# Kernel optimization log

Hardware: AMD Instinct MI355X
Metric: run time of the kernel (lower is better)

Reference implementation:

```python
import jax, jax.numpy as jnp
import numpy as np

PT_SEQ_LEN = 16    # hardcoded hw_seq_len in the module
THETA = 10000.0


def _rope_tables(head_dim):
    # VisionRotaryEmbeddingFast with dim = head_dim // 2, pt_seq_len = ft_seq_len = 16
    d = head_dim // 2                                   # 32
    freqs = 1.0 / (THETA ** (np.arange(0, d, 2, dtype=np.float64) / d))  # (d//2,) = (16,)
    t = np.arange(PT_SEQ_LEN, dtype=np.float64)         # t / ft * pt = arange since ft==pt
    f = np.einsum('i,j->ij', t, freqs)                  # (16, 16)
    f = np.repeat(f, 2, axis=-1)                        # (16, 32)  '... n -> ... (n r)'
    fa = np.broadcast_to(f[:, None, :], (PT_SEQ_LEN, PT_SEQ_LEN, d))
    fb = np.broadcast_to(f[None, :, :], (PT_SEQ_LEN, PT_SEQ_LEN, d))
    full = np.concatenate([fa, fb], axis=-1).reshape(-1, head_dim)  # (256, head_dim)
    return (jnp.asarray(np.cos(full), dtype=jnp.float32),
            jnp.asarray(np.sin(full), dtype=jnp.float32))


def _rotate_half(x):
    # '... (d r) -> ... d r', r=2; (x1, x2) -> (-x2, x1)
    x = x.reshape(*x.shape[:-1], -1, 2)
    x1, x2 = x[..., 0], x[..., 1]
    return jnp.stack((-x2, x1), axis=-1).reshape(*x.shape[:-2], -1)


def _apply_rope(t, cos, sin):
    # t: (B, H, N, hd); cos/sin: (N, hd)
    return t * cos + _rotate_half(t) * sin


def setup_inputs() -> dict:
    key = jax.random.key(0)
    ks = jax.random.split(key, 5)
    B, N, dim, sem = 64, 256, 1024, 768
    return {
        'q': jax.random.normal(ks[0], (B, N, dim), dtype=jnp.float32),
        'kv': jax.random.normal(ks[1], (B, N, sem), dtype=jnp.float32),
        'Wq': jax.random.normal(ks[2], (dim, dim), dtype=jnp.float32) * 0.02,
        'Wkv': jax.random.normal(ks[3], (sem, 2 * dim), dtype=jnp.float32) * 0.02,
        'Wproj': jax.random.normal(ks[4], (dim, dim), dtype=jnp.float32) * 0.02,
        'bproj': jnp.zeros((dim,), dtype=jnp.float32),
    }


def reference(q, kv, Wq, Wkv, Wproj, bproj):
    B, N, C = q.shape
    H = 16
    hd = C // H
    cos, sin = _rope_tables(hd)

    qh = (q @ Wq).reshape(B, N, H, hd).transpose(0, 2, 1, 3)        # (B,H,N,hd)
    kvh = (kv @ Wkv).reshape(B, N, 2, H, hd).transpose(2, 0, 3, 1, 4)
    k, v = kvh[0], kvh[1]                                           # (B,H,N,hd)

    qh = _apply_rope(qh, cos, sin)
    k = _apply_rope(k, cos, sin)

    scale = 1.0 / jnp.sqrt(jnp.float32(hd))  # F.sdpa default scale
    logits = jnp.einsum('bhqd,bhkd->bhqk', qh, k) * scale
    attn = jax.nn.softmax(logits, axis=-1)
    out = jnp.einsum('bhqk,bhkd->bhqd', attn, v)                    # (B,H,N,hd)
    out = out.transpose(0, 2, 1, 3).reshape(B, N, C)
    return out @ Wproj + bproj
```

## Files before the change

### kernel.cpp

```cpp
#include <hip/hip_runtime.h>
#include <hip/hip_bf16.h>
#include <math.h>


typedef unsigned int uint;
typedef __attribute__((ext_vector_type(4)))  short s16x4;
typedef __attribute__((ext_vector_type(8)))  short s16x8;
typedef __attribute__((ext_vector_type(4)))  float f32x4;
typedef __attribute__((ext_vector_type(16))) float f32x16;

#define AS1 __attribute__((address_space(1)))
#define AS3 __attribute__((address_space(3)))

__device__ __forceinline__ short f2bf(float x){
  union{float f;uint u;}v; v.f=x;
  return (short)((v.u + 0x7FFFu + ((v.u>>16)&1u))>>16);
}
__device__ __forceinline__ float bf2f(short s){
  union{float f;uint u;}v; v.u=((uint)(unsigned short)s)<<16; return v.f;
}
__device__ __forceinline__ uint packbf(float a,float b){
  return (uint)(unsigned short)f2bf(a) | ((uint)(unsigned short)f2bf(b)<<16);
}
__device__ __forceinline__ void gl_lds16(const void* g, void* l){
  __builtin_amdgcn_global_load_lds((const AS1 uint*)g, (AS3 uint*)l, 16, 0, 0);
}
__device__ __forceinline__ s16x8 ld16(const short* p){ return *(const s16x8*)p; }

__global__ void k_prep(const void* Wq, const void* Wkv, const void* Wp,
                       const void* bsrc, const void* qsrc, const void* kvsrc,
                       short* WqT, short* WkvT, short* WpT, float* biasF,
                       float* cosT, float* sinT, short* qbf, short* kvbf,
                       int* flag){
  __shared__ int cnt;
  const uint* qw=(const uint*)qsrc;
  if(threadIdx.x==0) cnt=0;
  __syncthreads();
  int c=0;
  for(int i=threadIdx.x;i<2048;i+=256){
    uint e=(qw[i]>>7)&0xFFu;
    if(e>=120u && e<=130u) c++;
  }
  atomicAdd(&cnt,c);
  __syncthreads();
  const int f=(cnt>1024)?0:1;
  if(threadIdx.x==0 && blockIdx.x==0) *flag=f;

  const long S0=16384, S1=S0+1024, S2=S1+131072, S3=S2+196608, S4=S3+131072,
             S5=S4+2097152, S6=S5+1572864;
  const long stride=(long)gridDim.x*blockDim.x;
  for(long idx=(long)blockIdx.x*blockDim.x+threadIdx.x; idx<S6; idx+=stride){
    if(idx<S0){
      int t=(int)idx, n=t>>6, d=t&63;
      int i=n>>4, j=n&15, p=(d&31)>>1;
      double fr=pow(10000.0, -(double)(2*p)/32.0);
      double tt=(d<32)?(double)i:(double)j;
      double a=tt*fr;
      cosT[t]=(float)cos(a); sinT[t]=(float)sin(a);
    } else if(idx<S1){
      int t=(int)(idx-S0);
      biasF[t]= f ? ((const float*)bsrc)[t] : bf2f(((const short*)bsrc)[t]);
    } else if(idx<S4){
      const void* W; short* WT; int K,Nn; long g;
      if(idx<S2){ W=Wq;  WT=WqT;  K=1024; Nn=1024; g=idx-S1; }
      else if(idx<S3){ W=Wkv; WT=WkvT; K=768; Nn=2048; g=idx-S2; }
      else { W=Wp;  WT=WpT;  K=1024; Nn=1024; g=idx-S3; }
      int n=(int)(g%Nn); int k0=(int)(g/Nn)*8;
      s16x8 o;
      #pragma unroll
      for(int j=0;j<8;j++){
        o[j]= f ? f2bf(((const float*)W)[(long)(k0+j)*Nn+n])
                : ((const short*)W)[(long)(k0+j)*Nn+n];
      }
      *(s16x8*)&WT[(long)n*K+k0]=o;
    } else {
      const void* src; short* dst; long i;
      if(idx<S5){ src=qsrc; dst=qbf; i=idx-S4; }
      else { src=kvsrc; dst=kvbf; i=idx-S5; }
      s16x8 o;
      if(f){
        const float4* s=(const float4*)src;
        float4 a=s[i*2], b=s[i*2+1];
        o[0]=f2bf(a.x);o[1]=f2bf(a.y);o[2]=f2bf(a.z);o[3]=f2bf(a.w);
        o[4]=f2bf(b.x);o[5]=f2bf(b.y);o[6]=f2bf(b.z);o[7]=f2bf(b.w);
      }else{
        o=((const s16x8*)src)[i];
      }
      ((s16x8*)dst)[i]=o;
    }
  }
}

#define BAR   __builtin_amdgcn_s_barrier()
#define LGKM0 asm volatile("s_waitcnt lgkmcnt(0)" ::: "memory")
#define VMC4  asm volatile("s_waitcnt vmcnt(4)" ::: "memory")
#define PRIO1 __builtin_amdgcn_s_setprio(1)
#define PRIO0 __builtin_amdgcn_s_setprio(0)

#define MM(H,V,BR) do{ \
  _Pragma("unroll") for(int ks_=0;ks_<4;ks_++){ \
    _Pragma("unroll") for(int mf_=0;mf_<2;mf_++){ \
      acc[(H)*2+mf_][V]=__builtin_amdgcn_mfma_f32_32x32x16_bf16( \
        aR[mf_][ks_],BR[ks_],acc[(H)*2+mf_][V],0,0,0); \
  }} }while(0)

#define HALFIT(BUF,TA,TB) do{ \
  const short* RA=&lds[BUF][0][wm][0]; \
  const short* RB=&lds[BUF][1][0][0]; \
  ldA(RA,0,aR); ldB(RB,0,bR0); stage(0,0,TA); \
  BAR; LGKM0; PRIO1; MM(0,0,bR0); PRIO0; BAR; \
  ldB(RB,1,bR1); stage(0,1,TA); \
  BAR; LGKM0; PRIO1; MM(0,1,bR1); PRIO0; BAR; \
  ldA(RA,1,aR); stage(1,0,TB); \
  BAR; LGKM0; PRIO1; MM(1,1,bR1); PRIO0; BAR; \
  stage(1,1,TB); \
  BAR; PRIO1; MM(1,0,bR0); PRIO0; VMC4; BAR; \
}while(0)

template<int MODE>
__launch_bounds__(512,2)
__global__ void k_gemm8(const short* __restrict__ Aq, const short* __restrict__ Bq,
                        const short* __restrict__ Akv, const short* __restrict__ Bkv,
                        short* __restrict__ out0, short* __restrict__ out1,
                        short* __restrict__ out2,
                        const float* __restrict__ cosT, const float* __restrict__ sinT,
                        const float* __restrict__ bias, const int* __restrict__ flag,
                        void* __restrict__ dout){
  __shared__ __align__(16) short lds[2][2][2][8192];
  const int tid=threadIdx.x, lane=tid&63, wave=tid>>6;
  const int ln31=lane&31, l5=lane>>5;
  const int wm=wave>>2, wn=wave&3;
  int role, tm, tn, Kdim;
  const short *Ag, *Bg;
  if(MODE==1){
    const int nwg=gridDim.x, cpx=nwg>>3;
    const int wg=((int)blockIdx.x&7)*cpx+((int)blockIdx.x>>3);
    role=2; tn=wg&3; tm=wg>>2; Kdim=1024;
    Ag=Aq+(long)tm*256*1024; Bg=Bq+(long)tn*256*1024;
  } else {
    const int xcd=(int)blockIdx.x&7, pos=(int)blockIdx.x>>3;
    if(pos<32){ role=0; int qi=xcd*32+pos; tn=qi&3; tm=qi>>2; Kdim=1024;
      Ag=Aq+(long)tm*256*1024; Bg=Bq+(long)tn*256*1024; }
    else { role=1; int ki=xcd*64+(pos-32); tn=ki&7; tm=ki>>3; Kdim=768;
      Ag=Akv+(long)tm*256*768; Bg=Bkv+(long)tn*256*768; }
  }
  const int NT=Kdim>>6;
  const int fl=(MODE==1)? *flag : 0;
  f32x16 acc[4][2]={};
  s16x8 aR[2][4], bR0[4], bR1[4];

  auto stage=[&](int op,int hf,int kt){
    int ktw=(kt>=NT)?kt-NT:kt;
    const short* G=(op? Bg:Ag)+((long)(hf*128))*Kdim+ktw*64;
    short* R=&lds[kt&1][op][hf][0];
    #pragma unroll
    for(int l=0;l<2;l++){
      int lr=l*64+wave*8+(lane>>3);
      int c=(lane&7)^((lr>>1)&7);
      gl_lds16(G+(long)lr*Kdim+c*8, R+l*4096+wave*512+lane*8);
    }
  };
  auto ldA=[&](const short* R,int h,s16x8 (&a)[2][4]){
    #pragma unroll
    for(int mf=0;mf<2;mf++){
      int lr=h*64+mf*32+ln31;
      int sw=(lr>>1)&7;
      #pragma unroll
      for(int ks=0;ks<4;ks++){
        int slot=(ks*2+l5)^sw;
        a[mf][ks]=*(const s16x8*)&R[lr*64+slot*8];
      }
    }
  };
  auto ldB=[&](const short* R0,int v,s16x8 (&b)[4]){
    int row=wn*64+v*32+ln31;
    const short* R=R0+(row>>7)*8192;
    int lr=row&127;
    int sw=(lr>>1)&7;
    #pragma unroll
    for(int ks=0;ks<4;ks++){
      int slot=(ks*2+l5)^sw;
      b[ks]=*(const s16x8*)&R[lr*64+slot*8];
    }
  };

  stage(1,0,0); stage(1,1,0); stage(0,0,0); stage(0,1,0);
  stage(1,0,1); stage(1,1,1);
  VMC4;
  BAR;

  for(int t=0;t<NT;t+=2){
    HALFIT(0, t+1, t+2);
    HALFIT(1, t+2, t+3);
  }

  const int mb=tm*256+wm*128, nb=tn*256+wn*64;
  #pragma unroll
  for(int mf=0;mf<4;mf++)
  #pragma unroll
  for(int nf=0;nf<2;nf++){
    const int n=nb+nf*32+ln31;
    if(MODE==1){
      float bi=bias[n];
      #pragma unroll
      for(int r=0;r<16;r++){
        int m=mb+mf*32+(r&3)+8*(r>>2)+4*l5;
        float o=acc[mf][nf][r]+bi;
        long idx=((long)m<<10)+n;
        if(fl) ((float*)dout)[idx]=o;
        else   ((short*)dout)[idx]=f2bf(o);
      }
    } else if(role==0){
      int h=n>>6, d=n&63;
      #pragma unroll
      for(int r=0;r<16;r++){
        int m=mb+mf*32+(r&3)+8*(r>>2)+4*l5;
        int b=m>>8, nn=m&255;
        float v=acc[mf][nf][r];
        float part=__shfl_xor(v,1);
        float c=cosT[(nn<<6)+d], s=sinT[(nn<<6)+d];
        float rot=(d&1)?part:-part;
        out0[(((long)(b*16+h)*256+nn)<<6)+d]=f2bf((v*c+rot*s)*0.125f);
      }
    } else {
      if(n<1024){
        int h=(n>>6)&15, d=n&63;
        #pragma unroll
        for(int r=0;r<16;r++){
          int m=mb+mf*32+(r&3)+8*(r>>2)+4*l5;
          int b=m>>8, nn=m&255;
          float v=acc[mf][nf][r];
          float part=__shfl_xor(v,1);
          float c=cosT[(nn<<6)+d], s=sinT[(nn<<6)+d];
          float rot=(d&1)?part:-part;
          out1[(((long)(b*16+h)*256+nn)<<6)+d]=f2bf(v*c+rot*s);
        }
      }else{
        int h=(n>>6)&15, d=n&63;
        #pragma unroll
        for(int rq=0;rq<4;rq++){
          int m0=mb+mf*32+8*rq+4*l5;
          int b=m0>>8, nn0=m0&255;
          s16x4 pk;
          #pragma unroll
          for(int j=0;j<4;j++) pk[j]=f2bf(acc[mf][nf][rq*4+j]);
          *(s16x4*)&out2[(((long)(b*16+h)*64+d)<<8)+nn0]=pk;
        }
      }
    }
  }
}

__launch_bounds__(256,2)
__global__ void k_attn(const short* qh, const short* kb, const short* vt, short* out){
  __shared__ __align__(16) short ol[4][64][72];
  int bh=blockIdx.x, b=bh>>4, h=bh&15;
  int tid=threadIdx.x, lane=tid&63, wave=tid>>6;
  const short* Q=qh+(long)bh*256*64;
  const short* K=kb+(long)bh*256*64;
  const short* VT=vt+(long)bh*64*256;

  s16x8 qf[4][2];
  #pragma unroll
  for(int qb=0;qb<4;qb++)
    #pragma unroll
    for(int kk=0;kk<2;kk++)
      qf[qb][kk]=ld16(Q+(wave*64+qb*16+(lane&15))*64+kk*32+(lane>>4)*8);

  f32x4 o[4][4]={};
  float mrow[4]={-INFINITY,-INFINITY,-INFINITY,-INFINITY};
  float srow[4]={0.f,0.f,0.f,0.f};
  const int g=lane>>4;
  const int srcA=(lane&15)|((((g<<1))&3)<<4);
  const int srcB=(lane&15)|((((g<<1)|1)&3)<<4);
  const bool hi=(g>=2);

  for(int kt=0;kt<8;kt++){
    s16x8 kA[2][2];
    #pragma unroll
    for(int f=0;f<2;f++)
      #pragma unroll
      for(int kk=0;kk<2;kk++)
        kA[f][kk]=ld16(K+(kt*32+f*16+(lane&15))*64+kk*32+(lane>>4)*8);
    s16x8 vA[4];
    #pragma unroll
    for(int db=0;db<4;db++)
      vA[db]=ld16(VT+(db*16+(lane&15))*256+kt*32+(lane>>4)*8);

    f32x4 st[2][4]={};
    PRIO1;
    #pragma unroll
    for(int kk=0;kk<2;kk++)
      #pragma unroll
      for(int f=0;f<2;f++)
        #pragma unroll
        for(int qb=0;qb<4;qb++)
          st[f][qb]=__builtin_amdgcn_mfma_f32_16x16x32_bf16(kA[f][kk],qf[qb][kk],st[f][qb],0,0,0);
    PRIO0;

    s16x8 pb[4];
    #pragma unroll
    for(int qb=0;qb<4;qb++){
      float pm=st[0][qb][0];
      #pragma unroll
      for(int f=0;f<2;f++)
        #pragma unroll
        for(int r=0;r<4;r++) pm=fmaxf(pm,st[f][qb][r]);
      pm=fmaxf(pm,__shfl_xor(pm,16));
      pm=fmaxf(pm,__shfl_xor(pm,32));
      float mn=fmaxf(mrow[qb],pm);
      float al=__expf(mrow[qb]-mn);
      mrow[qb]=mn;
      float p00=__expf(st[0][qb][0]-mn), p01=__expf(st[0][qb][1]-mn);
      float p02=__expf(st[0][qb][2]-mn), p03=__expf(st[0][qb][3]-mn);
      float p10=__expf(st[1][qb][0]-mn), p11=__expf(st[1][qb][1]-mn);
      float p12=__expf(st[1][qb][2]-mn), p13=__expf(st[1][qb][3]-mn);
      float ps=p00+p01+p02+p03+p10+p11+p12+p13;
      ps+=__shfl_xor(ps,16);
      ps+=__shfl_xor(ps,32);
      srow[qb]=srow[qb]*al+ps;
      #pragma unroll
      for(int db=0;db<4;db++){
        o[db][qb][0]*=al; o[db][qb][1]*=al; o[db][qb][2]*=al; o[db][qb][3]*=al;
      }
      uint pk00=packbf(p00,p01), pk01=packbf(p02,p03);
      uint pk10=packbf(p10,p11), pk11=packbf(p12,p13);
      uint s00=(uint)__shfl((int)pk00,srcA), s10=(uint)__shfl((int)pk10,srcA);
      uint s01=(uint)__shfl((int)pk01,srcA), s11=(uint)__shfl((int)pk11,srcA);
      uint t00=(uint)__shfl((int)pk00,srcB), t10=(uint)__shfl((int)pk10,srcB);
      uint t01=(uint)__shfl((int)pk01,srcB), t11=(uint)__shfl((int)pk11,srcB);
      union{s16x8 v;uint u[4];}pp;
      pp.u[0]=hi?s10:s00;
      pp.u[1]=hi?s11:s01;
      pp.u[2]=hi?t10:t00;
      pp.u[3]=hi?t11:t01;
      pb[qb]=pp.v;
    }
    PRIO1;
    #pragma unroll
    for(int db=0;db<4;db++)
      #pragma unroll
      for(int qb=0;qb<4;qb++)
        o[db][qb]=__builtin_amdgcn_mfma_f32_16x16x32_bf16(vA[db],pb[qb],o[db][qb],0,0,0);
    PRIO0;
  }

  #pragma unroll
  for(int db=0;db<4;db++)
    #pragma unroll
    for(int qb=0;qb<4;qb++)
      #pragma unroll
      for(int r=0;r<4;r++){
        int d=db*16+(lane>>4)*4+r;
        int q=qb*16+(lane&15);
        ol[wave][q][d]=f2bf(o[db][qb][r]/srow[qb]);
      }
  __syncthreads();
  #pragma unroll
  for(int it=0;it<8;it++){
    int q=wave*64+it*8+(lane>>3);
    int cc=lane&7;
    s16x8 x=*(const s16x8*)&ol[wave][it*8+(lane>>3)][cc*8];
    *(s16x8*)&out[((long)(b*256+q)<<10)+h*64+cc*8]=x;
  }
}

extern "C" void kernel_launch(void* const* d_in, const int* in_sizes, int n_in,
                              void* d_out, int out_size, void* d_ws, size_t ws_size,
                              hipStream_t stream){
  const long M=16384;
  char* ws=(char*)d_ws;
  size_t off=0;
  auto alloc=[&](size_t b){ void* p=ws+off; off+=(b+255)&~(size_t)255; return p; };
  int*   flag =(int*)  alloc(256);
  float* cosT =(float*)alloc(256*64*4);
  float* sinT =(float*)alloc(256*64*4);
  float* biasF=(float*)alloc(1024*4);
  short* qbf  =(short*)alloc((size_t)M*1024*2);
  short* kvbf =(short*)alloc((size_t)M*768*2);
  short* WqT  =(short*)alloc((size_t)1024*1024*2);
  short* WkvT =(short*)alloc((size_t)2048*768*2);
  short* WpT  =(short*)alloc((size_t)1024*1024*2);
  short* qhB  =(short*)alloc((size_t)16777216*2);
  short* kbuf =(short*)alloc((size_t)16777216*2);
  short* vtb  =(short*)alloc((size_t)16777216*2);

  k_prep<<<2048,256,0,stream>>>(d_in[2],d_in[3],d_in[4],d_in[5],d_in[0],d_in[1],
                                WqT,WkvT,WpT,biasF,cosT,sinT,qbf,kvbf,flag);
  k_gemm8<0><<<768,512,0,stream>>>(qbf,WqT,kvbf,WkvT,qhB,kbuf,vtb,
                                   cosT,sinT,biasF,flag,nullptr);
  k_attn<<<1024,256,0,stream>>>(qhB,kbuf,vtb,qbf);
  k_gemm8<1><<<256,512,0,stream>>>(qbf,WpT,nullptr,nullptr,nullptr,nullptr,nullptr,
                                   cosT,sinT,biasF,flag,d_out);
}
```

Baseline: 255.8 us.

## Specialize prep kernel blocks per task and add lazy softmax rescaling

The prep kernel drops its single grid-stride loop with per-element range branching and gives fixed block ranges to each job: RoPE tables and bias, weight transposes, and q/kv bf16 conversion. The dtype branch is hoisted out of the conversion loops. The attention inner loop now skips the running-max update and the rescaling of the output accumulator and row sum unless some lane's new tile max exceeds the stored max by more than 8, as in FA4-style lazy rescaling. This saves exps and multiplies per tile but assumes a launch of at least 2046 blocks, and exp values can grow up to e^8 before normalization.

```diff
diff --git a/kernel.cpp b/kernel.cpp
--- a/kernel.cpp
+++ b/kernel.cpp
@@ -46,25 +46,24 @@
   const int f=(cnt>1024)?0:1;
   if(threadIdx.x==0 && blockIdx.x==0) *flag=f;
 
-  const long S0=16384, S1=S0+1024, S2=S1+131072, S3=S2+196608, S4=S3+131072,
-             S5=S4+2097152, S6=S5+1572864;
-  const long stride=(long)gridDim.x*blockDim.x;
-  for(long idx=(long)blockIdx.x*blockDim.x+threadIdx.x; idx<S6; idx+=stride){
-    if(idx<S0){
-      int t=(int)idx, n=t>>6, d=t&63;
-      int i=n>>4, j=n&15, p=(d&31)>>1;
+  const int bid=blockIdx.x, tid=threadIdx.x;
+  if(bid<8){
+    const int t0=bid*256+tid;
+    for(int t=t0;t<16384;t+=2048){
+      int n=t>>6, d=t&63, i=n>>4, j=n&15, p=(d&31)>>1;
       double fr=pow(10000.0, -(double)(2*p)/32.0);
       double tt=(d<32)?(double)i:(double)j;
       double a=tt*fr;
       cosT[t]=(float)cos(a); sinT[t]=(float)sin(a);
-    } else if(idx<S1){
-      int t=(int)(idx-S0);
-      biasF[t]= f ? ((const float*)bsrc)[t] : bf2f(((const short*)bsrc)[t]);
-    } else if(idx<S4){
-      const void* W; short* WT; int K,Nn; long g;
-      if(idx<S2){ W=Wq;  WT=WqT;  K=1024; Nn=1024; g=idx-S1; }
-      else if(idx<S3){ W=Wkv; WT=WkvT; K=768; Nn=2048; g=idx-S2; }
-      else { W=Wp;  WT=WpT;  K=1024; Nn=1024; g=idx-S3; }
+    }
+    if(t0<1024)
+      biasF[t0]= f ? ((const float*)bsrc)[t0] : bf2f(((const short*)bsrc)[t0]);
+  } else if(bid<134){
+    const void* W; short* WT; int K,Nn; long base,total,nthr;
+    if(bid<44){ W=Wq;  WT=WqT;  K=1024; Nn=1024; base=(long)(bid-8)*256+tid;  total=131072; nthr=36*256; }
+    else if(bid<98){ W=Wkv; WT=WkvT; K=768; Nn=2048; base=(long)(bid-44)*256+tid; total=196608; nthr=54*256; }
+    else { W=Wp;  WT=WpT;  K=1024; Nn=1024; base=(long)(bid-98)*256+tid; total=131072; nthr=36*256; }
+    for(long g=base; g<total; g+=nthr){
       int n=(int)(g%Nn); int k0=(int)(g/Nn)*8;
       s16x8 o;
       #pragma unroll
@@ -73,20 +72,23 @@
                 : ((const short*)W)[(long)(k0+j)*Nn+n];
       }
       *(s16x8*)&WT[(long)n*K+k0]=o;
-    } else {
-      const void* src; short* dst; long i;
-      if(idx<S5){ src=qsrc; dst=qbf; i=idx-S4; }
-      else { src=kvsrc; dst=kvbf; i=idx-S5; }
-      s16x8 o;
-      if(f){
-        const float4* s=(const float4*)src;
+    }
+  } else if(bid<2046){
+    const void* src; short* dst; long base,total,nthr;
+    if(bid<1226){ src=qsrc;  dst=qbf;  base=(long)(bid-134)*256+tid;  total=2097152; nthr=1092L*256; }
+    else        { src=kvsrc; dst=kvbf; base=(long)(bid-1226)*256+tid; total=1572864; nthr=820L*256;  }
+    if(f){
+      const float4* s=(const float4*)src;
+      for(long i=base;i<total;i+=nthr){
         float4 a=s[i*2], b=s[i*2+1];
+        s16x8 o;
         o[0]=f2bf(a.x);o[1]=f2bf(a.y);o[2]=f2bf(a.z);o[3]=f2bf(a.w);
         o[4]=f2bf(b.x);o[5]=f2bf(b.y);o[6]=f2bf(b.z);o[7]=f2bf(b.w);
-      }else{
-        o=((const s16x8*)src)[i];
-      }
-      ((s16x8*)dst)[i]=o;
+        ((s16x8*)dst)[i]=o;
+      }
+    }else{
+      for(long i=base;i<total;i+=nthr)
+        ((s16x8*)dst)[i]=((const s16x8*)src)[i];
     }
   }
 }
@@ -308,9 +310,17 @@
         for(int r=0;r<4;r++) pm=fmaxf(pm,st[f][qb][r]);
       pm=fmaxf(pm,__shfl_xor(pm,16));
       pm=fmaxf(pm,__shfl_xor(pm,32));
-      float mn=fmaxf(mrow[qb],pm);
-      float al=__expf(mrow[qb]-mn);
-      mrow[qb]=mn;
+      if(!__all(pm-mrow[qb]<=8.f)){
+        float mn=fmaxf(mrow[qb],pm);
+        float al=__expf(mrow[qb]-mn);
+        mrow[qb]=mn;
+        srow[qb]*=al;
+        #pragma unroll
+        for(int db=0;db<4;db++){
+          o[db][qb][0]*=al; o[db][qb][1]*=al; o[db][qb][2]*=al; o[db][qb][3]*=al;
+        }
+      }
+      const float mn=mrow[qb];
       float p00=__expf(st[0][qb][0]-mn), p01=__expf(st[0][qb][1]-mn);
       float p02=__expf(st[0][qb][2]-mn), p03=__expf(st[0][qb][3]-mn);
       float p10=__expf(st[1][qb][0]-mn), p11=__expf(st[1][qb][1]-mn);
@@ -318,11 +328,7 @@
       float ps=p00+p01+p02+p03+p10+p11+p12+p13;
       ps+=__shfl_xor(ps,16);
       ps+=__shfl_xor(ps,32);
-      srow[qb]=srow[qb]*al+ps;
-      #pragma unroll
-      for(int db=0;db<4;db++){
-        o[db][qb][0]*=al; o[db][qb][1]*=al; o[db][qb][2]*=al; o[db][qb][3]*=al;
-      }
+      srow[qb]+=ps;
       uint pk00=packbf(p00,p01), pk01=packbf(p02,p03);
       uint pk10=packbf(p10,p11), pk11=packbf(p12,p13);
       uint s00=(uint)__shfl((int)pk00,srcA), s10=(uint)__shfl((int)pk10,srcA);
```

Result: slower. 279.0 us (+9.1%).
